# Performance work log

Measured on AMD Instinct MI355X. Metric: run time of the kernel, lower is better.

The kernel has to match this reference:

```python
import jax, jax.numpy as jnp
import numpy as np

N_IMG, N_CAP, N_REG, N_WORD = 64, 64, 36, 20
EMBED, SIM = 1024, 256
RCAR_STEP = 3          # rar_step=3, rcr_step=2, alv_step=3
T2I_SMOOTH = 9.0
EPS = 1e-8


def l2norm(x):
    return x / (jnp.linalg.norm(x, axis=-1, keepdims=True) + EPS)


def xavier(key, shape):
    fan_in, fan_out = shape[-1], shape[-2]
    r = float(np.sqrt(6.0 / (fan_in + fan_out)))
    return jax.random.uniform(key, shape, jnp.float32, -r, r)


def cross_attention(query, context, matrix, smooth):
    # query: (B, Q, D), context: (B, S, D); matrix broadcasts over query; smooth scalar or (B,Q,1)
    q = query * matrix
    attn = jnp.einsum('bsd,bqd->bsq', context, q)          # (B, S, Q)
    attn = jax.nn.leaky_relu(attn, 0.1)
    attn = l2norm(attn)                                     # normalize over Q
    attn = jnp.swapaxes(attn, 1, 2)                         # (B, Q, S)
    attn = jax.nn.softmax(attn * smooth, axis=2)
    wcontext = jnp.einsum('bqs,bsd->bqd', attn, context)    # (B, Q, D)
    return l2norm(wcontext)


def setup_inputs() -> dict:
    key = jax.random.key(0)
    ks = jax.random.split(key, 12)
    inp = {}
    inp['img_emb'] = jax.random.normal(ks[0], (N_IMG, N_REG, EMBED), jnp.float32)
    inp['cap_emb'] = jax.random.normal(ks[1], (N_CAP, N_WORD, EMBED), jnp.float32)
    inp['cap_lens'] = jnp.full((N_CAP,), N_WORD, dtype=jnp.int32)
    # Alignment_vector: Linear(embed -> sim), 3 steps
    inp['alv_w'] = xavier(ks[2], (RCAR_STEP, SIM, EMBED))
    inp['alv_b'] = jnp.zeros((RCAR_STEP, SIM), jnp.float32)
    # Aggregation_regulator: q/k Linear(sim->sim), v Linear(sim->1), 3 steps
    inp['rar_qw'] = xavier(ks[3], (RCAR_STEP, SIM, SIM))
    inp['rar_qb'] = jnp.zeros((RCAR_STEP, SIM), jnp.float32)
    inp['rar_kw'] = xavier(ks[4], (RCAR_STEP, SIM, SIM))
    inp['rar_kb'] = jnp.zeros((RCAR_STEP, SIM), jnp.float32)
    inp['rar_vw'] = xavier(ks[5], (RCAR_STEP, 1, SIM))
    inp['rar_vb'] = jnp.zeros((RCAR_STEP, 1), jnp.float32)
    # Correpondence_regulator: smooth MLP sim->sim//2->1, matrix MLP sim->2*sim->embed, 2 steps
    inp['rcr_sw1'] = xavier(ks[6], (RCAR_STEP - 1, SIM // 2, SIM))
    inp['rcr_sb1'] = jnp.zeros((RCAR_STEP - 1, SIM // 2), jnp.float32)
    inp['rcr_sw2'] = xavier(ks[7], (RCAR_STEP - 1, 1, SIM // 2))
    inp['rcr_sb2'] = jnp.zeros((RCAR_STEP - 1, 1), jnp.float32)
    inp['rcr_mw1'] = xavier(ks[8], (RCAR_STEP - 1, 2 * SIM, SIM))
    inp['rcr_mb1'] = jnp.zeros((RCAR_STEP - 1, 2 * SIM), jnp.float32)
    inp['rcr_mw2'] = xavier(ks[9], (RCAR_STEP - 1, EMBED, 2 * SIM))
    inp['rcr_mb2'] = jnp.zeros((RCAR_STEP - 1, EMBED), jnp.float32)
    # sim_eval_w: Linear(sim -> 1)
    inp['eval_w'] = xavier(ks[10], (1, SIM))
    inp['eval_b'] = jnp.zeros((1,), jnp.float32)
    return inp


def _forward(img_emb, cap_emb,
             alv_w, alv_b,
             rar_qw, rar_qb, rar_kw, rar_kb, rar_vw, rar_vb,
             rcr_sw1, rcr_sb1, rcr_sw2, rcr_sb2, rcr_mw1, rcr_mb1, rcr_mw2, rcr_mb2,
             eval_w, eval_b):
    n_img = img_emb.shape[0]

    def per_caption(cap_i):                       # cap_i: (L, D)
        query = jnp.broadcast_to(cap_i[None], (n_img,) + cap_i.shape)  # t2i: text is query
        context = img_emb                                               # (n_img, S, D)
        matrix = jnp.ones((EMBED,), cap_i.dtype)
        smooth = jnp.asarray(T2I_SMOOTH, cap_i.dtype)
        sim_hig = None
        for m in range(RCAR_STEP):
            # Alignment_vector (dropout is inference-mode identity)
            wctx = cross_attention(query, context, matrix, smooth)
            sim_rep = (query - wctx) ** 2
            sim_mid = l2norm(jnp.einsum('bqd,sd->bqs', sim_rep, alv_w[m]) + alv_b[m])  # (B,Q,SIM)
            if m == 0:
                sim_hig = sim_mid.mean(axis=1)                                          # (B,SIM)
            if m < RCAR_STEP - 1:
                # Correpondence_regulator
                hm = jnp.tanh(jnp.einsum('bqs,ts->bqt', sim_mid, rcr_mw1[m]) + rcr_mb1[m])
                mm = jnp.einsum('bqt,dt->bqd', hm, rcr_mw2[m]) + rcr_mb2[m]
                matrix = jnp.clip(jnp.tanh(mm) + matrix, -1.0, 1.0)                     # (B,Q,D)
                hs = jnp.tanh(jnp.einsum('bqs,ts->bqt', sim_mid, rcr_sw1[m]) + rcr_sb1[m])
                ss = jnp.einsum('bqt,ot->bqo', hs, rcr_sw2[m]) + rcr_sb2[m]
                smooth = jax.nn.relu(ss + smooth)                                       # (B,Q,1)
            # Aggregation_regulator
            mid_k = jnp.tanh(jnp.einsum('bqs,ts->bqt', sim_mid, rar_kw[m]) + rar_kb[m])
            hig_q = jnp.tanh(sim_hig @ rar_qw[m].T + rar_qb[m])[:, None, :]             # (B,1,SIM)
            w = jnp.einsum('bqs,os->bqo', mid_k * hig_q, rar_vw[m]) + rar_vb[m]         # (B,Q,1)
            w = jax.nn.softmax(w[..., 0], axis=1)
            sim_hig = l2norm(jnp.einsum('bq,bqs->bs', w, sim_mid))
        sim_i = jax.nn.sigmoid(sim_hig @ eval_w.T + eval_b)                             # (B,1)
        return sim_i[:, 0]

    sims = jax.vmap(per_caption)(cap_emb)        # (n_cap, n_img)
    return sims.T                                 # (n_img, n_cap) == torch.cat(sim_all, 1)


def reference(img_emb, cap_emb, cap_lens,
              alv_w, alv_b,
              rar_qw, rar_qb, rar_kw, rar_kb, rar_vw, rar_vb,
              rcr_sw1, rcr_sb1, rcr_sw2, rcr_sb2, rcr_mw1, rcr_mb1, rcr_mw2, rcr_mb2,
              eval_w, eval_b):
    # cap_lens are all equal to N_WORD (constant-length captions), so the per-caption
    # slice cap_emb[i, :n_word] is the full row and the loop vectorizes exactly.
    del cap_lens
    return _forward(img_emb, cap_emb, alv_w, alv_b,
                    rar_qw, rar_qb, rar_kw, rar_kb, rar_vw, rar_vb,
                    rcr_sw1, rcr_sb1, rcr_sw2, rcr_sb2, rcr_mw1, rcr_mb1, rcr_mw2, rcr_mb2,
                    eval_w, eval_b)
```

## Files before the change

### kernel.cpp

```cpp
#include <hip/hip_runtime.h>
#include <math.h>

#define NIMG 64
#define NCAP 64
#define NREG 36
#define NWORD 20
#define EMBED 1024
#define SIMDIM 256
#define H1 512
#define HSD 128
#define EPS 1e-8f

#define QSTR 1032
#define SMSTR 264
#define PSTR 72
#define ATSTR 37

typedef unsigned short u16t;
typedef __bf16 bf8 __attribute__((ext_vector_type(8)));
typedef short  s8i __attribute__((ext_vector_type(8)));
typedef float  f4  __attribute__((ext_vector_type(4)));

__device__ __forceinline__ float wsum(float v) {
#pragma unroll
  for (int o = 32; o > 0; o >>= 1) v += __shfl_xor(v, o);
  return v;
}
__device__ __forceinline__ float wmax(float v) {
#pragma unroll
  for (int o = 32; o > 0; o >>= 1) v = fmaxf(v, __shfl_xor(v, o));
  return v;
}
__device__ __forceinline__ float ftanh(float x) {
  x = fminf(fmaxf(x, -15.f), 15.f);
  float e = __expf(2.f * x);
  return (e - 1.f) / (e + 1.f);
}
__device__ __forceinline__ float d4(float4 a, float4 b) {
  return a.x*b.x + a.y*b.y + a.z*b.z + a.w*b.w;
}
__device__ __forceinline__ u16t f2bf(float f) {
  unsigned u = __float_as_uint(f);
  u += 0x7FFFu + ((u >> 16) & 1u);
  return (u16t)(u >> 16);
}
__device__ __forceinline__ float bf2f(u16t h) { return __uint_as_float(((unsigned)h) << 16); }
__device__ __forceinline__ bf8 zero8() {
  s8i z = {0,0,0,0,0,0,0,0};
  return __builtin_bit_cast(bf8, z);
}
#define MFMA16(a, b, c) __builtin_amdgcn_mfma_f32_16x16x32_bf16((a), (b), (c), 0, 0, 0)

#define WS_ALV   0u
#define WS_KW    786432u
#define WS_MW1   983040u
#define WS_MW2   1245184u
#define WS_SW1   2293760u
#define WS_IMG   2359296u
#define WS_CTXT  4718592u
#define WS_END   8912896u
#define N_CVT    4718592u

#define OFFB_MAT    17825792ull
#define OFFB_SMID   (OFFB_MAT + 83886080ull)
#define OFFB_SHIG   (OFFB_SMID + 41943040ull)
#define OFFB_SMOOTH (OFFB_SHIG + 4194304ull)
#define WS_FULL_BYTES (OFFB_SMOOTH + 327680ull)

__global__ void cvt_kernel(const float* __restrict__ alv, const float* __restrict__ kw,
                           const float* __restrict__ mw1, const float* __restrict__ mw2,
                           const float* __restrict__ sw1, const float* __restrict__ img,
                           u16t* __restrict__ ws) {
  for (unsigned i = blockIdx.x * blockDim.x + threadIdx.x; i < N_CVT; i += gridDim.x * blockDim.x) {
    unsigned o = i; float v;
    if (o < 786432u) v = alv[o];
    else if ((o -= 786432u) < 196608u) v = kw[o];
    else if ((o -= 196608u) < 262144u) v = mw1[o];
    else if ((o -= 262144u) < 1048576u) v = mw2[o];
    else if ((o -= 1048576u) < 65536u) v = sw1[o];
    else { o -= 65536u; v = img[o]; }
    ws[i] = f2bf(v);
  }
}

__global__ void ctxt_kernel(const float* __restrict__ img, u16t* __restrict__ ctxT) {
  __shared__ float tile[36 * 65];
  int b = blockIdx.x;
  int im = b >> 4, dt = (b & 15) * 64;
  const float* src = img + (size_t)im * 36 * 1024 + dt;
  for (int e = threadIdx.x; e < 36 * 64; e += 256) {
    int s = e >> 6, dd = e & 63;
    tile[s * 65 + dd] = src[s * 1024 + dd];
  }
  __syncthreads();
  u16t* dst = ctxT + (size_t)im * 65536 + dt * 64;
  for (int o = threadIdx.x; o < 4096; o += 256) {
    int dd = o >> 6, sp = o & 63;
    dst[dd * 64 + sp] = (sp < 36) ? f2bf(tile[sp * 65 + dd]) : (u16t)0;
  }
}

__global__ __launch_bounds__(512, 4) void simenc_k1(
    const float* __restrict__ cap_emb,
    const float* __restrict__ alv_b,
    const float* __restrict__ rar_qw, const float* __restrict__ rar_qb,
    const float* __restrict__ rar_kb,
    const float* __restrict__ rar_vw, const float* __restrict__ rar_vb,
    const float* __restrict__ sb1, const float* __restrict__ sw2, const float* __restrict__ sb2,
    const float* __restrict__ eval_w, const float* __restrict__ eval_b,
    const u16t* __restrict__ ws,
    signed char* __restrict__ mat_g, u16t* __restrict__ smid_g,
    float* __restrict__ shig_g, float* __restrict__ smooth_g,
    int m, float* __restrict__ out)
{
  __shared__ __attribute__((aligned(16))) u16t qsrep[NWORD * QSTR];
  __shared__ __attribute__((aligned(16))) u16t smidb[NWORD * SMSTR];
  __shared__ __attribute__((aligned(16))) u16t p_bf[NWORD * PSTR];
  __shared__ float attnT[NWORD * ATSTR];
  __shared__ float colscale[36];
  __shared__ float smoothq[NWORD];
  __shared__ float sim_hig[SIMDIM];
  __shared__ float red[8 * NWORD];
  __shared__ float rq[NWORD];
  __shared__ float logits_s[NWORD];
  __shared__ float wsm[NWORD];
  __shared__ float ssig_s;

  const int tid = threadIdx.x;
  const int lane = tid & 63;
  const int wv = tid >> 6;
  const int lr = lane & 15;
  const int lg = lane >> 4;
  const int koff = lg * 8;

  const int xcd = blockIdx.x & 7;
  const int j_  = blockIdx.x >> 3;
  const int img = xcd * 8 + (j_ & 7);
  const int cap = j_ >> 3;
  const int pid = img * NCAP + cap;

  const float* qry  = cap_emb + (size_t)cap * (NWORD * EMBED);
  const u16t* imgW  = ws + WS_IMG + (size_t)img * (NREG * EMBED);
  const u16t* ctxTW = ws + WS_CTXT + (size_t)img * (EMBED * 64);
  const u16t* alvW  = ws + WS_ALV + (size_t)m * (SIMDIM * EMBED);
  const u16t* kwW   = ws + WS_KW  + (size_t)m * (SIMDIM * SIMDIM);
  const u16t* sw1W  = ws + WS_SW1 + (size_t)m * (HSD * SIMDIM);

  if (tid < NWORD)
    smoothq[tid] = (m == 0) ? 9.0f : smooth_g[(size_t)pid * 20 + tid];
  if (m > 0 && tid < 256)
    sim_hig[tid] = shig_g[(size_t)pid * 256 + tid];
  __syncthreads();

  if (m == 0) {
#pragma unroll 4
    for (int q = 0; q < NWORD; ++q) {
      qsrep[q * QSTR + tid] = f2bf(qry[q * 1024 + tid]);
      qsrep[q * QSTR + 512 + tid] = f2bf(qry[q * 1024 + 512 + tid]);
    }
  } else {
    const signed char* mg = mat_g + (size_t)pid * 20480;
#pragma unroll 4
    for (int q = 0; q < NWORD; ++q) {
      float mv0 = (float)mg[q * 1024 + tid] * (1.f / 127.f);
      float mv1 = (float)mg[q * 1024 + 512 + tid] * (1.f / 127.f);
      qsrep[q * QSTR + tid] = f2bf(qry[q * 1024 + tid] * mv0);
      qsrep[q * QSTR + 512 + tid] = f2bf(qry[q * 1024 + 512 + tid] * mv1);
    }
  }
  __syncthreads();

  if (wv < 6) {
    int q0 = (wv & 1) * 16, s0 = (wv >> 1) * 16;
    int ari = q0 + lr; bool am = ari >= NWORD; int ar = am ? 0 : ari;
    int bri = s0 + lr; bool bm = bri >= NREG;  int br = bm ? 0 : bri;
    const u16t* ap = qsrep + ar * QSTR + koff;
    const u16t* bp = imgW + (size_t)br * 1024 + koff;
    f4 acc0 = {0.f,0.f,0.f,0.f}, acc1 = {0.f,0.f,0.f,0.f};
#pragma unroll 2
    for (int kk = 0; kk < 32; kk += 2) {
      bf8 a0 = *(const bf8*)(ap + kk * 32);       if (am) a0 = zero8();
      bf8 b0 = *(const bf8*)(bp + kk * 32);       if (bm) b0 = zero8();
      bf8 a1 = *(const bf8*)(ap + (kk + 1) * 32); if (am) a1 = zero8();
      bf8 b1 = *(const bf8*)(bp + (kk + 1) * 32); if (bm) b1 = zero8();
      acc0 = MFMA16(a0, b0, acc0);
      acc1 = MFMA16(a1, b1, acc1);
    }
    f4 acc = acc0 + acc1;
#pragma unroll
    for (int r = 0; r < 4; ++r) {
      int q = q0 + lg * 4 + r, s = s0 + lr;
      if (q < NWORD && s < NREG) {
        float x = acc[r];
        attnT[q * ATSTR + s] = (x > 0.f) ? x : 0.1f * x;
      }
    }
  }
  __syncthreads();

  if (tid < NREG) {
    float ss = 0.f;
#pragma unroll
    for (int q = 0; q < NWORD; ++q) { float v = attnT[q * ATSTR + tid]; ss += v * v; }
    colscale[tid] = 1.f / (sqrtf(ss) + EPS);
  }
  __syncthreads();

#pragma unroll
  for (int pass = 0; pass < 3; ++pass) {
    int q = wv + pass * 8;
    if (q < NWORD) {
      float x = (lane < NREG)
              ? attnT[q * ATSTR + lane] * colscale[lane] * smoothq[q] : -1e30f;
      float mx = wmax(x);
      float e = (lane < NREG) ? __expf(x - mx) : 0.f;
      float s = wsum(e);
      p_bf[q * PSTR + lane] = f2bf(e / s);
    }
  }
  __syncthreads();

  {
    bf8 pa[2][2];
#pragma unroll
    for (int kk = 0; kk < 2; ++kk) {
      pa[0][kk] = *(const bf8*)(p_bf + lr * PSTR + kk * 32 + koff);
      pa[1][kk] = (16 + lr < NWORD)
                ? *(const bf8*)(p_bf + (16 + lr) * PSTR + kk * 32 + koff) : zero8();
    }
    float s2[8];
#pragma unroll
    for (int i = 0; i < 8; ++i) s2[i] = 0.f;
#pragma unroll
    for (int nt = 0; nt < 8; ++nt) {
      int d0 = wv * 128 + nt * 16;
      const u16t* bp = ctxTW + (size_t)(d0 + lr) * 64 + koff;
      bf8 b0 = *(const bf8*)(bp);
      bf8 b1 = *(const bf8*)(bp + 32);
      int d = d0 + lr;
#pragma unroll
      for (int m2 = 0; m2 < 2; ++m2) {
        f4 acc = {0.f,0.f,0.f,0.f};
        acc = MFMA16(pa[m2][0], b0, acc);
        acc = MFMA16(pa[m2][1], b1, acc);
#pragma unroll
        for (int r = 0; r < 4; ++r) {
          int q = m2 * 16 + lg * 4 + r;
          s2[m2 * 4 + r] += acc[r] * acc[r];
          if (q < NWORD) qsrep[q * QSTR + d] = f2bf(acc[r]);
        }
      }
    }
#pragma unroll
    for (int o = 1; o < 16; o <<= 1)
#pragma unroll
      for (int i = 0; i < 8; ++i) s2[i] += __shfl_xor(s2[i], o);
    if (lr == 0) {
#pragma unroll
      for (int r = 0; r < 4; ++r) red[wv * 20 + lg * 4 + r] = s2[r];
      if (lg == 0)
#pragma unroll
        for (int r = 0; r < 4; ++r) red[wv * 20 + 16 + r] = s2[4 + r];
    }
    __syncthreads();
    if (tid < NWORD) {
      float s = 0.f;
#pragma unroll
      for (int w = 0; w < 8; ++w) s += red[w * 20 + tid];
      rq[tid] = 1.f / (sqrtf(s) + EPS);
    }
    __syncthreads();
#pragma unroll
    for (int nt = 0; nt < 8; ++nt) {
      int d = wv * 128 + nt * 16 + lr;
#pragma unroll
      for (int m2 = 0; m2 < 2; ++m2)
#pragma unroll
        for (int r = 0; r < 4; ++r) {
          int q = m2 * 16 + lg * 4 + r;
          if (q < NWORD) {
            float wn = bf2f(qsrep[q * QSTR + d]) * rq[q];
            float t = qry[q * 1024 + d] - wn;
            qsrep[q * QSTR + d] = f2bf(t * t);
          }
        }
    }
  }
  __syncthreads();

  {
    int t0 = wv * 32 + lr;
    const u16t* bp0 = alvW + (size_t)t0 * 1024 + koff;
    const u16t* bp1 = bp0 + 16 * 1024;
    int ari = 16 + lr; bool am = ari >= NWORD; int ar = am ? 0 : ari;
    f4 a00 = {0,0,0,0}, a01 = {0,0,0,0}, a10 = {0,0,0,0}, a11 = {0,0,0,0};
#pragma unroll 2
    for (int kk = 0; kk < 32; ++kk) {
      bf8 b0 = *(const bf8*)(bp0 + kk * 32);
      bf8 b1 = *(const bf8*)(bp1 + kk * 32);
      bf8 x0 = *(const bf8*)(qsrep + lr * QSTR + kk * 32 + koff);
      bf8 x1 = *(const bf8*)(qsrep + ar * QSTR + kk * 32 + koff); if (am) x1 = zero8();
      a00 = MFMA16(x0, b0, a00);
      a01 = MFMA16(x1, b0, a01);
      a10 = MFMA16(x0, b1, a10);
      a11 = MFMA16(x1, b1, a11);
    }
    float bias0 = alv_b[m * SIMDIM + t0];
    float bias1 = alv_b[m * SIMDIM + t0 + 16];
    float s2[8];
#pragma unroll
    for (int r = 0; r < 4; ++r) {
      a00[r] += bias0; a10[r] += bias1;
      s2[r] = a00[r] * a00[r] + a10[r] * a10[r];
    }
#pragma unroll
    for (int r = 0; r < 4; ++r) {
      a01[r] += bias0; a11[r] += bias1;
      s2[4 + r] = (lg == 0) ? a01[r] * a01[r] + a11[r] * a11[r] : 0.f;
    }
#pragma unroll
    for (int o = 1; o < 16; o <<= 1)
#pragma unroll
      for (int i = 0; i < 8; ++i) s2[i] += __shfl_xor(s2[i], o);
    if (lr == 0) {
#pragma unroll
      for (int r = 0; r < 4; ++r) red[wv * 20 + lg * 4 + r] = s2[r];
      if (lg == 0)
#pragma unroll
        for (int r = 0; r < 4; ++r) red[wv * 20 + 16 + r] = s2[4 + r];
    }
    __syncthreads();
    if (tid < NWORD) {
      float s = 0.f;
#pragma unroll
      for (int w = 0; w < 8; ++w) s += red[w * 20 + tid];
      rq[tid] = 1.f / (sqrtf(s) + EPS);
    }
    __syncthreads();
    u16t* sg = smid_g + (size_t)pid * 5120;
#pragma unroll
    for (int r = 0; r < 4; ++r) {
      int q = lg * 4 + r;
      float v0 = a00[r] * rq[q], v1 = a10[r] * rq[q];
      u16t h0 = f2bf(v0), h1 = f2bf(v1);
      ((float*)(qsrep + q * QSTR + 512))[t0] = v0;
      ((float*)(qsrep + q * QSTR + 512))[t0 + 16] = v1;
      smidb[q * SMSTR + t0] = h0;
      smidb[q * SMSTR + t0 + 16] = h1;
      sg[q * 256 + t0] = h0;
      sg[q * 256 + t0 + 16] = h1;
    }
    if (lg == 0)
#pragma unroll
      for (int r = 0; r < 4; ++r) {
        int q = 16 + r;
        float v0 = a01[r] * rq[q], v1 = a11[r] * rq[q];
        u16t h0 = f2bf(v0), h1 = f2bf(v1);
        ((float*)(qsrep + q * QSTR + 512))[t0] = v0;
        ((float*)(qsrep + q * QSTR + 512))[t0 + 16] = v1;
        smidb[q * SMSTR + t0] = h0;
        smidb[q * SMSTR + t0 + 16] = h1;
        sg[q * 256 + t0] = h0;
        sg[q * 256 + t0 + 16] = h1;
      }
  }
  __syncthreads();

  if (m == 0 && tid < 256) {
    float s = 0.f;
#pragma unroll
    for (int q = 0; q < NWORD; ++q) s += ((const float*)(qsrep + q * QSTR + 512))[tid];
    sim_hig[tid] = s * (1.f / NWORD);
  }
  __syncthreads();

  if (m < 2) {
    {
      int j0 = wv * 16;
      int ari = 16 + lr; bool am = ari >= NWORD; int ar = am ? 0 : ari;
      f4 h0 = {0,0,0,0}, h1 = {0,0,0,0};
#pragma unroll 2
      for (int kk = 0; kk < 8; ++kk) {
        bf8 b = *(const bf8*)(sw1W + (size_t)(j0 + lr) * 256 + kk * 32 + koff);
        bf8 x0 = *(const bf8*)(smidb + lr * SMSTR + kk * 32 + koff);
        bf8 x1 = *(const bf8*)(smidb + ar * SMSTR + kk * 32 + koff); if (am) x1 = zero8();
        h0 = MFMA16(x0, b, h0);
        h1 = MFMA16(x1, b, h1);
      }
      int j = j0 + lr;
      float bias = sb1[m * HSD + j];
      float s2v = sw2[m * HSD + j];
      float part[8];
#pragma unroll
      for (int r = 0; r < 4; ++r) part[r] = ftanh(h0[r] + bias) * s2v;
#pragma unroll
      for (int r = 0; r < 4; ++r) part[4 + r] = (lg == 0) ? ftanh(h1[r] + bias) * s2v : 0.f;
#pragma unroll
      for (int o = 1; o < 16; o <<= 1)
#pragma unroll
        for (int i = 0; i < 8; ++i) part[i] += __shfl_xor(part[i], o);
      if (lr == 0) {
#pragma unroll
        for (int r = 0; r < 4; ++r) red[wv * 20 + lg * 4 + r] = part[r];
        if (lg == 0)
#pragma unroll
          for (int r = 0; r < 4; ++r) red[wv * 20 + 16 + r] = part[4 + r];
      }
    }
    __syncthreads();
    if (tid < NWORD) {
      float s = 0.f;
#pragma unroll
      for (int w = 0; w < 8; ++w) s += red[w * 20 + tid];
      smooth_g[(size_t)pid * 20 + tid] = fmaxf(0.f, s + sb2[m] + smoothq[tid]);
    }
    __syncthreads();
  }

  {
    int ari = 16 + lr; bool am = ari >= NWORD; int ar = am ? 0 : ari;
    float part[8];
#pragma unroll
    for (int i = 0; i < 8; ++i) part[i] = 0.f;
#pragma unroll
    for (int h = 0; h < 2; ++h) {
      int t_ = wv * 32 + h * 16 + lr;
      const float4* wq = (const float4*)(rar_qw + ((size_t)m * SIMDIM + t_) * SIMDIM);
      const float4* sh = (const float4*)sim_hig;
      float hacc = 0.f;
#pragma unroll 2
      for (int i = 0; i < SIMDIM / 4; ++i) hacc += d4(wq[i], sh[i]);
      float hq = ftanh(hacc + rar_qb[m * SIMDIM + t_]) * rar_vw[m * SIMDIM + t_];

      f4 k0 = {0,0,0,0}, k1v = {0,0,0,0};
#pragma unroll 2
      for (int kk = 0; kk < 8; ++kk) {
        bf8 b = *(const bf8*)(kwW + (size_t)t_ * 256 + kk * 32 + koff);
        bf8 x0 = *(const bf8*)(smidb + lr * SMSTR + kk * 32 + koff);
        bf8 x1 = *(const bf8*)(smidb + ar * SMSTR + kk * 32 + koff); if (am) x1 = zero8();
        k0 = MFMA16(x0, b, k0);
        k1v = MFMA16(x1, b, k1v);
      }
      float kb = rar_kb[m * SIMDIM + t_];
#pragma unroll
      for (int r = 0; r < 4; ++r) part[r] += ftanh(k0[r] + kb) * hq;
      if (lg == 0)
#pragma unroll
        for (int r = 0; r < 4; ++r) part[4 + r] += ftanh(k1v[r] + kb) * hq;
    }
#pragma unroll
    for (int o = 1; o < 16; o <<= 1)
#pragma unroll
      for (int i = 0; i < 8; ++i) part[i] += __shfl_xor(part[i], o);
    if (lr == 0) {
#pragma unroll
      for (int r = 0; r < 4; ++r) red[wv * 20 + lg * 4 + r] = part[r];
      if (lg == 0)
#pragma unroll
        for (int r = 0; r < 4; ++r) red[wv * 20 + 16 + r] = part[4 + r];
    }
  }
  __syncthreads();
  if (tid < NWORD) {
    float s = 0.f;
#pragma unroll
    for (int w = 0; w < 8; ++w) s += red[w * 20 + tid];
    logits_s[tid] = s + rar_vb[m];
  }
  __syncthreads();
  if (tid < 64) {
    float v = (tid < NWORD) ? logits_s[tid] : -1e30f;
    float mx = wmax(v);
    float e = (tid < NWORD) ? __expf(v - mx) : 0.f;
    float s = wsum(e);
    if (tid < NWORD) wsm[tid] = e / s;
  }
  __syncthreads();
  if (tid < 256) {
    float a = 0.f;
#pragma unroll
    for (int q = 0; q < NWORD; ++q) a += wsm[q] * ((const float*)(qsrep + q * QSTR + 512))[tid];
    sim_hig[tid] = a;
  }
  __syncthreads();
  if (tid < 64) {
    float4 v = ((const float4*)sim_hig)[tid];
    float s = wsum(d4(v, v));
    if (tid == 0) ssig_s = 1.f / (sqrtf(s) + EPS);
  }
  __syncthreads();

  if (m < 2) {
    if (tid < 256)
      shig_g[(size_t)pid * 256 + tid] = sim_hig[tid] * ssig_s;
  } else {
    if (tid < 64) {
      float4 s4v = ((const float4*)sim_hig)[tid];
      float4 w4v = ((const float4*)eval_w)[tid];
      float v = wsum(d4(s4v, w4v)) * ssig_s;
      if (tid == 0)
        out[pid] = 1.f / (1.f + __expf(-(v + eval_b[0])));
    }
  }
}

__global__ __launch_bounds__(1024, 4) void simenc_k2(
    const float* __restrict__ mb1, const float* __restrict__ mb2,
    const u16t* __restrict__ ws,
    const u16t* __restrict__ smid_g, signed char* __restrict__ mat_g,
    int m)
{
  __shared__ __attribute__((aligned(16))) u16t hm_l[80 * 512];
  __shared__ __attribute__((aligned(16))) signed char mat_l[80 * 1024];

  const int tid = threadIdx.x;
  const int lane = tid & 63;
  const int wv = tid >> 6;
  const int lr = lane & 15;
  const int lg = lane >> 4;
  const int koff = lg * 8;

  const int pid0 = blockIdx.x * 4;
  const u16t* mw1W = ws + WS_MW1 + (size_t)m * (H1 * SIMDIM);
  const u16t* mw2W = ws + WS_MW2 + (size_t)m * (EMBED * H1);
  const u16t* smidB = smid_g + (size_t)pid0 * 5120;

#pragma unroll
  for (int nt = 0; nt < 2; ++nt) {
    int j0 = (wv * 2 + nt) * 16;
    f4 acc[5];
#pragma unroll
    for (int mt = 0; mt < 5; ++mt) acc[mt] = (f4){0,0,0,0};
#pragma unroll 2
    for (int kk = 0; kk < 8; ++kk) {
      bf8 b = *(const bf8*)(mw1W + (size_t)(j0 + lr) * 256 + kk * 32 + koff);
#pragma unroll
      for (int mt = 0; mt < 5; ++mt) {
        bf8 a = *(const bf8*)(smidB + (size_t)(mt * 16 + lr) * 256 + kk * 32 + koff);
        acc[mt] = MFMA16(a, b, acc[mt]);
      }
    }
    int j = j0 + lr;
    float bias = mb1[m * H1 + j];
#pragma unroll
    for (int mt = 0; mt < 5; ++mt)
#pragma unroll
      for (int r = 0; r < 4; ++r) {
        int rb = mt * 16 + lg * 4 + r;
        unsigned byteoff = (unsigned)rb * 1024u
                         + (((unsigned)j * 2u) ^ (((unsigned)rb & 7u) << 4));
        *(u16t*)((char*)hm_l + byteoff) = f2bf(ftanh(acc[mt][r] + bias));
      }
  }
  __syncthreads();

#pragma unroll
  for (int nt = 0; nt < 4; ++nt) {
    int d0 = (wv * 4 + nt) * 16;
    f4 acc[5];
#pragma unroll
    for (int mt = 0; mt < 5; ++mt) acc[mt] = (f4){0,0,0,0};
#pragma unroll 2
    for (int kk = 0; kk < 16; ++kk) {
      bf8 b = *(const bf8*)(mw2W + (size_t)(d0 + lr) * 512 + kk * 32 + koff);
#pragma unroll
      for (int mt = 0; mt < 5; ++mt) {
        int rb = mt * 16 + lr;
        unsigned byteoff = (unsigned)rb * 1024u
                         + (((unsigned)(kk * 64 + lg * 16)) ^ (((unsigned)rb & 7u) << 4));
        bf8 a = *(const bf8*)((const char*)hm_l + byteoff);
        acc[mt] = MFMA16(a, b, acc[mt]);
      }
    }
    int d = d0 + lr;
    float bias = mb2[m * EMBED + d];
#pragma unroll
    for (int mt = 0; mt < 5; ++mt)
#pragma unroll
      for (int r = 0; r < 4; ++r) {
        int rb = mt * 16 + lg * 4 + r;
        float v = ftanh(acc[mt][r] + bias);
        mat_l[rb * 1024 + d] = (signed char)__float2int_rn(v * 127.f);
      }
  }
  __syncthreads();

  {
    signed char* matB = mat_g + (size_t)pid0 * 20480;
#pragma unroll
    for (int i = 0; i < 5; ++i) {
      int off = i * 16384 + tid * 16;
      int4 sv = *(const int4*)(mat_l + off);
      int4 ov;
      if (m > 0) ov = *(const int4*)(matB + off);
      const signed char* svb = (const signed char*)&sv;
      const signed char* ovb = (const signed char*)&ov;
      int4 res;
      signed char* rsb = (signed char*)&res;
#pragma unroll
      for (int b = 0; b < 16; ++b) {
        float v = (float)svb[b] * (1.f / 127.f);
        float mo = (m == 0) ? 1.f : (float)ovb[b] * (1.f / 127.f);
        float mn = fminf(fmaxf(v + mo, -1.f), 1.f);
        rsb[b] = (signed char)__float2int_rn(mn * 127.f);
      }
      *(int4*)(matB + off) = res;
    }
  }
}

__global__ __launch_bounds__(1024) void simenc_valu(
    const float* __restrict__ img_emb, const float* __restrict__ cap_emb,
    const float* __restrict__ alv_w,  const float* __restrict__ alv_b,
    const float* __restrict__ rar_qw, const float* __restrict__ rar_qb,
    const float* __restrict__ rar_kw, const float* __restrict__ rar_kb,
    const float* __restrict__ rar_vw, const float* __restrict__ rar_vb,
    const float* __restrict__ sw1, const float* __restrict__ sb1,
    const float* __restrict__ sw2, const float* __restrict__ sb2,
    const float* __restrict__ mw1, const float* __restrict__ mb1,
    const float* __restrict__ mw2, const float* __restrict__ mb2,
    const float* __restrict__ eval_w, const float* __restrict__ eval_b,
    float* __restrict__ out)
{
  __shared__ float buf[NWORD * EMBED];
  __shared__ float smid[NWORD * SIMDIM];
  __shared__ float attn_raw[NREG * NWORD];
  __shared__ float attnT[NWORD * NREG];
  __shared__ float smoothq[NWORD];
  __shared__ float sim_hig[SIMDIM];
  __shared__ float hqu[SIMDIM];
  __shared__ float wsm_[NWORD];
  __shared__ float red[16 * NWORD];
  __shared__ float rq[NWORD];
  __shared__ float ssig;

  const int tid = threadIdx.x;
  const int lane = tid & 63;
  const int wv = tid >> 6;
  const int pair = blockIdx.x;
  const int img = pair & 63;
  const int cap = pair >> 6;
  const float* ctx = img_emb + (size_t)img * (NREG * EMBED);
  const float* qry = cap_emb + (size_t)cap * (NWORD * EMBED);

  float mat[NWORD];
#pragma unroll
  for (int q = 0; q < NWORD; ++q) mat[q] = 1.f;
  if (tid < NWORD) smoothq[tid] = 9.f;
  __syncthreads();

  for (int m = 0; m < 3; ++m) {
#pragma unroll 4
    for (int q = 0; q < NWORD; ++q)
      buf[q * EMBED + tid] = qry[q * EMBED + tid] * mat[q];
    __syncthreads();
    if (tid < NWORD * NREG) {
      int q = tid / NREG, s = tid % NREG;
      const float4* c4 = (const float4*)(ctx + s * EMBED);
      const float4* q4 = (const float4*)(buf + q * EMBED);
      float acc = 0.f;
#pragma unroll 4
      for (int i = 0; i < EMBED / 4; ++i) acc += d4(c4[i], q4[i]);
      attn_raw[s * NWORD + q] = (acc > 0.f) ? acc : 0.1f * acc;
    }
    __syncthreads();
    if (tid < NREG) {
      int s = tid; float sumsq = 0.f;
#pragma unroll
      for (int q = 0; q < NWORD; ++q) { float v = attn_raw[s * NWORD + q]; sumsq += v * v; }
      float sc = 1.f / (sqrtf(sumsq) + EPS);
#pragma unroll
      for (int q = 0; q < NWORD; ++q) attnT[q * NREG + s] = attn_raw[s * NWORD + q] * sc;
    }
    __syncthreads();
    if (tid < NWORD) {
      int q = tid; float sm = smoothq[q]; float mx = -1e30f;
      for (int s = 0; s < NREG; ++s) mx = fmaxf(mx, attnT[q * NREG + s] * sm);
      float sum = 0.f;
      for (int s = 0; s < NREG; ++s) { float e = __expf(attnT[q * NREG + s] * sm - mx); attnT[q * NREG + s] = e; sum += e; }
      float r = 1.f / sum;
      for (int s = 0; s < NREG; ++s) attnT[q * NREG + s] *= r;
    }
    __syncthreads();
    {
      float wacc[NWORD];
#pragma unroll
      for (int q = 0; q < NWORD; ++q) wacc[q] = 0.f;
#pragma unroll
      for (int sc_ = 0; sc_ < 3; ++sc_) {
        float c[12];
#pragma unroll
        for (int i = 0; i < 12; ++i) c[i] = ctx[(sc_ * 12 + i) * EMBED + tid];
#pragma unroll
        for (int q = 0; q < NWORD; ++q) {
          const float4* a4 = (const float4*)(attnT + q * NREG + sc_ * 12);
          float4 a0 = a4[0], a1 = a4[1], a2 = a4[2];
          wacc[q] += a0.x*c[0] + a0.y*c[1] + a0.z*c[2] + a0.w*c[3]
                   + a1.x*c[4] + a1.y*c[5] + a1.z*c[6] + a1.w*c[7]
                   + a2.x*c[8] + a2.y*c[9] + a2.z*c[10] + a2.w*c[11];
        }
      }
#pragma unroll
      for (int q = 0; q < NWORD; ++q) {
        float v = wsum(wacc[q] * wacc[q]);
        if (lane == 0) red[wv * NWORD + q] = v;
      }
      __syncthreads();
      if (tid < NWORD) {
        float s = 0.f;
#pragma unroll
        for (int w = 0; w < 16; ++w) s += red[w * NWORD + tid];
        rq[tid] = 1.f / (sqrtf(s) + EPS);
      }
      __syncthreads();
#pragma unroll 4
      for (int q = 0; q < NWORD; ++q) {
        float wn = wacc[q] * rq[q];
        float t = qry[q * EMBED + tid] - wn;
        buf[q * EMBED + tid] = t * t;
      }
    }
    __syncthreads();
    {
      int t = tid & 255, g = tid >> 8;
      const float4* w4 = (const float4*)(alv_w + ((size_t)m * SIMDIM + t) * EMBED);
      float acc[5] = {0, 0, 0, 0, 0};
      for (int i = 0; i < EMBED / 4; ++i) {
        float4 w = w4[i];
#pragma unroll
        for (int k = 0; k < 5; ++k) acc[k] += d4(w, ((const float4*)(buf + (g + 4 * k) * EMBED))[i]);
      }
      float b = alv_b[m * SIMDIM + t];
#pragma unroll
      for (int k = 0; k < 5; ++k) smid[(g + 4 * k) * SIMDIM + t] = acc[k] + b;
    }
    __syncthreads();
#pragma unroll
    for (int rep = 0; rep < 2; ++rep) {
      int q = wv + rep * 16;
      if (q < NWORD) {
        float4 v = ((const float4*)(smid + q * SIMDIM))[lane];
        float s = wsum(d4(v, v));
        if (lane == 0) rq[q] = 1.f / (sqrtf(s) + EPS);
      }
    }
    __syncthreads();
#pragma unroll
    for (int k = 0; k < 5; ++k) { int e = tid + k * 1024; smid[e] *= rq[e >> 8]; }
    __syncthreads();
    if (m == 0 && tid < SIMDIM) {
      float s = 0.f;
#pragma unroll
      for (int q = 0; q < NWORD; ++q) s += smid[q * SIMDIM + tid];
      sim_hig[tid] = s * (1.f / NWORD);
    }
    __syncthreads();
    if (m < 2) {
      {
        int j = tid & 511, g = tid >> 9;
        const float4* w4 = (const float4*)(mw1 + ((size_t)m * H1 + j) * SIMDIM);
        float acc[10];
#pragma unroll
        for (int k = 0; k < 10; ++k) acc[k] = 0.f;
        for (int i = 0; i < SIMDIM / 4; ++i) {
          float4 w = w4[i];
#pragma unroll
          for (int k = 0; k < 10; ++k) acc[k] += d4(w, ((const float4*)(smid + (g + 2 * k) * SIMDIM))[i]);
        }
        float b = mb1[m * H1 + j];
#pragma unroll
        for (int k = 0; k < 10; ++k) buf[(g + 2 * k) * H1 + j] = ftanh(acc[k] + b);
      }
      __syncthreads();
      {
        const float4* w4 = (const float4*)(mw2 + ((size_t)m * EMBED + tid) * H1);
        float acc[NWORD];
#pragma unroll
        for (int q = 0; q < NWORD; ++q) acc[q] = 0.f;
        for (int i = 0; i < H1 / 4; ++i) {
          float4 w = w4[i];
#pragma unroll
          for (int q = 0; q < NWORD; ++q) acc[q] += d4(w, ((const float4*)(buf + q * H1))[i]);
        }
        float b = mb2[m * EMBED + tid];
#pragma unroll
        for (int q = 0; q < NWORD; ++q)
          mat[q] = fminf(fmaxf(ftanh(acc[q] + b) + mat[q], -1.f), 1.f);
      }
      {
        int j = tid & 127, g = tid >> 7;
        const float4* w4 = (const float4*)(sw1 + ((size_t)m * HSD + j) * SIMDIM);
        float a0 = 0.f, a1 = 0.f, a2 = 0.f;
        for (int i = 0; i < SIMDIM / 4; ++i) {
          float4 w = w4[i];
          a0 += d4(w, ((const float4*)(smid + g * SIMDIM))[i]);
          a1 += d4(w, ((const float4*)(smid + (g + 8) * SIMDIM))[i]);
          if (g < 4) a2 += d4(w, ((const float4*)(smid + (g + 16) * SIMDIM))[i]);
        }
        float b = sb1[m * HSD + j];
        buf[10240 + g * HSD + j] = ftanh(a0 + b);
        buf[10240 + (g + 8) * HSD + j] = ftanh(a1 + b);
        if (g < 4) buf[10240 + (g + 16) * HSD + j] = ftanh(a2 + b);
      }
      __syncthreads();
      {
        const float* sw2m = sw2 + m * HSD;
#pragma unroll
        for (int rep = 0; rep < 2; ++rep) {
          int q = wv + rep * 16;
          if (q < NWORD) {
            float v = buf[10240 + q * HSD + lane] * sw2m[lane]
                    + buf[10240 + q * HSD + 64 + lane] * sw2m[64 + lane];
            v = wsum(v);
            if (lane == 0) smoothq[q] = fmaxf(0.f, v + sb2[m] + smoothq[q]);
          }
        }
      }
      __syncthreads();
    }
    {
      int t = tid & 255, g = tid >> 8;
      const float4* w4 = (const float4*)(rar_kw + ((size_t)m * SIMDIM + t) * SIMDIM);
      float acc[5] = {0, 0, 0, 0, 0};
      for (int i = 0; i < SIMDIM / 4; ++i) {
        float4 w = w4[i];
#pragma unroll
        for (int k = 0; k < 5; ++k) acc[k] += d4(w, ((const float4*)(smid + (g + 4 * k) * SIMDIM))[i]);
      }
      float b = rar_kb[m * SIMDIM + t];
#pragma unroll
      for (int k = 0; k < 5; ++k) buf[12800 + (g + 4 * k) * SIMDIM + t] = ftanh(acc[k] + b);
    }
    if (tid < SIMDIM) {
      const float4* w4 = (const float4*)(rar_qw + ((size_t)m * SIMDIM + tid) * SIMDIM);
      const float4* s4 = (const float4*)sim_hig;
      float acc = 0.f;
      for (int i = 0; i < SIMDIM / 4; ++i) acc += d4(w4[i], s4[i]);
      hqu[tid] = ftanh(acc + rar_qb[m * SIMDIM + tid]) * rar_vw[m * SIMDIM + tid];
    }
    __syncthreads();
#pragma unroll
    for (int rep = 0; rep < 2; ++rep) {
      int q = wv + rep * 16;
      if (q < NWORD) {
        float4 a = ((const float4*)(buf + 12800 + q * SIMDIM))[lane];
        float4 u = ((const float4*)hqu)[lane];
        float v = wsum(d4(a, u));
        if (lane == 0) red[q] = v + rar_vb[m];
      }
    }
    __syncthreads();
    if (tid < 64) {
      float v = (tid < NWORD) ? red[tid] : -1e30f;
      float mx = wmax(v);
      float e = (tid < NWORD) ? __expf(v - mx) : 0.f;
      float s = wsum(e);
      if (tid < NWORD) wsm_[tid] = e / s;
    }
    __syncthreads();
    if (tid < SIMDIM) {
      float acc = 0.f;
#pragma unroll
      for (int q = 0; q < NWORD; ++q) acc += wsm_[q] * smid[q * SIMDIM + tid];
      sim_hig[tid] = acc;
    }
    __syncthreads();
    if (tid < 64) {
      float4 v = ((const float4*)sim_hig)[tid];
      float s = wsum(d4(v, v));
      if (tid == 0) ssig = 1.f / (sqrtf(s) + EPS);
    }
    __syncthreads();
    if (tid < SIMDIM) sim_hig[tid] *= ssig;
    __syncthreads();
  }
  if (tid < 64) {
    float4 s4v = ((const float4*)sim_hig)[tid];
    float4 w4v = ((const float4*)eval_w)[tid];
    float v = wsum(d4(s4v, w4v));
    if (tid == 0) out[img * NCAP + cap] = 1.f / (1.f + __expf(-(v + eval_b[0])));
  }
}

extern "C" void kernel_launch(void* const* d_in, const int* in_sizes, int n_in,
                              void* d_out, int out_size, void* d_ws, size_t ws_size,
                              hipStream_t stream) {
  (void)in_sizes; (void)n_in; (void)out_size;
  u16t* ws = (u16t*)d_ws;

  if (ws_size >= (size_t)WS_FULL_BYTES) {
    cvt_kernel<<<2048, 1024, 0, stream>>>(
        (const float*)d_in[3],  (const float*)d_in[7],  (const float*)d_in[15],
        (const float*)d_in[17], (const float*)d_in[11], (const float*)d_in[0], ws);
    ctxt_kernel<<<1024, 256, 0, stream>>>((const float*)d_in[0], ws + WS_CTXT);

    signed char* mat_g = (signed char*)d_ws + OFFB_MAT;
    u16t*  smid_g   = (u16t*)((char*)d_ws + OFFB_SMID);
    float* shig_g   = (float*)((char*)d_ws + OFFB_SHIG);
    float* smooth_g = (float*)((char*)d_ws + OFFB_SMOOTH);

    for (int m = 0; m < 3; ++m) {
      simenc_k1<<<NIMG * NCAP, 512, 0, stream>>>(
          (const float*)d_in[1],  (const float*)d_in[4],
          (const float*)d_in[5],  (const float*)d_in[6],  (const float*)d_in[8],
          (const float*)d_in[9],  (const float*)d_in[10],
          (const float*)d_in[12], (const float*)d_in[13], (const float*)d_in[14],
          (const float*)d_in[19], (const float*)d_in[20],
          ws, mat_g, smid_g, shig_g, smooth_g, m, (float*)d_out);
      if (m < 2)
        simenc_k2<<<NIMG * NCAP / 4, 1024, 0, stream>>>(
            (const float*)d_in[16], (const float*)d_in[18],
            ws, smid_g, mat_g, m);
    }
  } else {
    simenc_valu<<<NIMG * NCAP, 1024, 0, stream>>>(
        (const float*)d_in[0],  (const float*)d_in[1],
        (const float*)d_in[3],  (const float*)d_in[4],
        (const float*)d_in[5],  (const float*)d_in[6],
        (const float*)d_in[7],  (const float*)d_in[8],
        (const float*)d_in[9],  (const float*)d_in[10],
        (const float*)d_in[11], (const float*)d_in[12],
        (const float*)d_in[13], (const float*)d_in[14],
        (const float*)d_in[15], (const float*)d_in[16],
        (const float*)d_in[17], (const float*)d_in[18],
        (const float*)d_in[19], (const float*)d_in[20],
        (float*)d_out);
  }
}
```

Measured before the change: 3.517 ms.

## Split per-pair encoder kernel into staged kernels batching weight GEMMs across pairs

The monolithic per-(image,caption) kernel is split into stages. An attention kernel writes the squared-difference representation to global memory. A batched kernel then applies the alignment linear layer with MFMA over four pairs per block, followed by separate kernels for the query projection, key/smooth projections, and softmax aggregation. This amortizes weight loads across pairs and raises MFMA tile utilization. In exchange it adds about 160 MB of extra global traffic per step for the intermediate buffer, plus more kernel launches. The old fallback VALU kernel is removed in favour of the previous fused path.

```diff
diff --git a/kernel.cpp b/kernel.cpp
--- a/kernel.cpp
+++ b/kernel.cpp
@@ -66,6 +66,10 @@
 #define OFFB_SHIG   (OFFB_SMID + 41943040ull)
 #define OFFB_SMOOTH (OFFB_SHIG + 4194304ull)
 #define WS_FULL_BYTES (OFFB_SMOOTH + 327680ull)
+#define OFFB_SREP   (OFFB_SMOOTH + 327680ull)
+#define OFFB_HQU    (OFFB_SREP + 167772160ull)
+#define OFFB_LOG    (OFFB_HQU + 4194304ull)
+#define WS_FULL2_BYTES (OFFB_LOG + 327680ull)
 
 __global__ void cvt_kernel(const float* __restrict__ alv, const float* __restrict__ kw,
                            const float* __restrict__ mw1, const float* __restrict__ mw2,
@@ -100,7 +104,551 @@
   }
 }
 
-__global__ __launch_bounds__(512, 4) void simenc_k1(
+__global__ __launch_bounds__(512, 4) void simenc_ka(
+    const float* __restrict__ cap_emb,
+    const u16t* __restrict__ ws,
+    const signed char* __restrict__ mat_g,
+    const float* __restrict__ smooth_g,
+    u16t* __restrict__ srep_g,
+    int m)
+{
+  __shared__ __attribute__((aligned(16))) u16t qsrep[NWORD * QSTR];
+  __shared__ __attribute__((aligned(16))) u16t p_bf[NWORD * PSTR];
+  __shared__ float attnT[NWORD * ATSTR];
+  __shared__ float colscale[36];
+  __shared__ float smoothq[NWORD];
+  __shared__ float red[8 * NWORD];
+  __shared__ float rq[NWORD];
+
+  const int tid = threadIdx.x;
+  const int lane = tid & 63;
+  const int wv = tid >> 6;
+  const int lr = lane & 15;
+  const int lg = lane >> 4;
+  const int koff = lg * 8;
+
+  const int xcd = blockIdx.x & 7;
+  const int j_  = blockIdx.x >> 3;
+  const int img = xcd * 8 + (j_ & 7);
+  const int cap = j_ >> 3;
+  const int pid = img * NCAP + cap;
+
+  const float* qry  = cap_emb + (size_t)cap * (NWORD * EMBED);
+  const u16t* imgW  = ws + WS_IMG + (size_t)img * (NREG * EMBED);
+  const u16t* ctxTW = ws + WS_CTXT + (size_t)img * (EMBED * 64);
+
+  if (tid < NWORD)
+    smoothq[tid] = (m == 0) ? 9.0f : smooth_g[(size_t)pid * 20 + tid];
+  __syncthreads();
+
+  if (m == 0) {
+#pragma unroll 4
+    for (int q = 0; q < NWORD; ++q) {
+      qsrep[q * QSTR + tid] = f2bf(qry[q * 1024 + tid]);
+      qsrep[q * QSTR + 512 + tid] = f2bf(qry[q * 1024 + 512 + tid]);
+    }
+  } else {
+    const signed char* mg = mat_g + (size_t)pid * 20480;
+#pragma unroll 4
+    for (int q = 0; q < NWORD; ++q) {
+      float mv0 = (float)mg[q * 1024 + tid] * (1.f / 127.f);
+      float mv1 = (float)mg[q * 1024 + 512 + tid] * (1.f / 127.f);
+      qsrep[q * QSTR + tid] = f2bf(qry[q * 1024 + tid] * mv0);
+      qsrep[q * QSTR + 512 + tid] = f2bf(qry[q * 1024 + 512 + tid] * mv1);
+    }
+  }
+  __syncthreads();
+
+  if (wv < 6) {
+    int q0 = (wv & 1) * 16, s0 = (wv >> 1) * 16;
+    int ari = q0 + lr; bool am = ari >= NWORD; int ar = am ? 0 : ari;
+    int bri = s0 + lr; bool bm = bri >= NREG;  int br = bm ? 0 : bri;
+    const u16t* ap = qsrep + ar * QSTR + koff;
+    const u16t* bp = imgW + (size_t)br * 1024 + koff;
+    f4 acc0 = {0.f,0.f,0.f,0.f}, acc1 = {0.f,0.f,0.f,0.f};
+#pragma unroll 2
+    for (int kk = 0; kk < 32; kk += 2) {
+      bf8 a0 = *(const bf8*)(ap + kk * 32);       if (am) a0 = zero8();
+      bf8 b0 = *(const bf8*)(bp + kk * 32);       if (bm) b0 = zero8();
+      bf8 a1 = *(const bf8*)(ap + (kk + 1) * 32); if (am) a1 = zero8();
+      bf8 b1 = *(const bf8*)(bp + (kk + 1) * 32); if (bm) b1 = zero8();
+      acc0 = MFMA16(a0, b0, acc0);
+      acc1 = MFMA16(a1, b1, acc1);
+    }
+    f4 acc = acc0 + acc1;
+#pragma unroll
+    for (int r = 0; r < 4; ++r) {
+      int q = q0 + lg * 4 + r, s = s0 + lr;
+      if (q < NWORD && s < NREG) {
+        float x = acc[r];
+        attnT[q * ATSTR + s] = (x > 0.f) ? x : 0.1f * x;
+      }
+    }
+  }
+  __syncthreads();
+
+  if (tid < NREG) {
+    float ss = 0.f;
+#pragma unroll
+    for (int q = 0; q < NWORD; ++q) { float v = attnT[q * ATSTR + tid]; ss += v * v; }
+    colscale[tid] = 1.f / (sqrtf(ss) + EPS);
+  }
+  __syncthreads();
+
+#pragma unroll
+  for (int pass = 0; pass < 3; ++pass) {
+    int q = wv + pass * 8;
+    if (q < NWORD) {
+      float x = (lane < NREG)
+              ? attnT[q * ATSTR + lane] * colscale[lane] * smoothq[q] : -1e30f;
+      float mx = wmax(x);
+      float e = (lane < NREG) ? __expf(x - mx) : 0.f;
+      float s = wsum(e);
+      p_bf[q * PSTR + lane] = f2bf(e / s);
+    }
+  }
+  __syncthreads();
+
+  {
+    bf8 pa[2][2];
+#pragma unroll
+    for (int kk = 0; kk < 2; ++kk) {
+      pa[0][kk] = *(const bf8*)(p_bf + lr * PSTR + kk * 32 + koff);
+      pa[1][kk] = (16 + lr < NWORD)
+                ? *(const bf8*)(p_bf + (16 + lr) * PSTR + kk * 32 + koff) : zero8();
+    }
+    float s2[8];
+#pragma unroll
+    for (int i = 0; i < 8; ++i) s2[i] = 0.f;
+#pragma unroll
+    for (int nt = 0; nt < 8; ++nt) {
+      int d0 = wv * 128 + nt * 16;
+      const u16t* bp = ctxTW + (size_t)(d0 + lr) * 64 + koff;
+      bf8 b0 = *(const bf8*)(bp);
+      bf8 b1 = *(const bf8*)(bp + 32);
+      int d = d0 + lr;
+#pragma unroll
+      for (int m2 = 0; m2 < 2; ++m2) {
+        f4 acc = {0.f,0.f,0.f,0.f};
+        acc = MFMA16(pa[m2][0], b0, acc);
+        acc = MFMA16(pa[m2][1], b1, acc);
+#pragma unroll
+        for (int r = 0; r < 4; ++r) {
+          int q = m2 * 16 + lg * 4 + r;
+          s2[m2 * 4 + r] += acc[r] * acc[r];
+          if (q < NWORD) qsrep[q * QSTR + d] = f2bf(acc[r]);
+        }
+      }
+    }
+#pragma unroll
+    for (int o = 1; o < 16; o <<= 1)
+#pragma unroll
+      for (int i = 0; i < 8; ++i) s2[i] += __shfl_xor(s2[i], o);
+    if (lr == 0) {
+#pragma unroll
+      for (int r = 0; r < 4; ++r) red[wv * 20 + lg * 4 + r] = s2[r];
+      if (lg == 0)
+#pragma unroll
+        for (int r = 0; r < 4; ++r) red[wv * 20 + 16 + r] = s2[4 + r];
+    }
+    __syncthreads();
+    if (tid < NWORD) {
+      float s = 0.f;
+#pragma unroll
+      for (int w = 0; w < 8; ++w) s += red[w * 20 + tid];
+      rq[tid] = 1.f / (sqrtf(s) + EPS);
+    }
+    __syncthreads();
+#pragma unroll
+    for (int nt = 0; nt < 8; ++nt) {
+      int d = wv * 128 + nt * 16 + lr;
+#pragma unroll
+      for (int m2 = 0; m2 < 2; ++m2)
+#pragma unroll
+        for (int r = 0; r < 4; ++r) {
+          int q = m2 * 16 + lg * 4 + r;
+          if (q < NWORD) {
+            float wn = bf2f(qsrep[q * QSTR + d]) * rq[q];
+            float t = qry[q * 1024 + d] - wn;
+            qsrep[q * QSTR + d] = f2bf(t * t);
+          }
+        }
+    }
+  }
+  __syncthreads();
+
+  {
+    u16t* sp = srep_g + (size_t)pid * 20480;
+#pragma unroll 4
+    for (int i = tid; i < 20480; i += 512) {
+      int row = i >> 10, col = i & 1023;
+      sp[i] = qsrep[row * QSTR + col];
+    }
+  }
+}
+
+__global__ __launch_bounds__(1024, 4) void simenc_kf(
+    const float* __restrict__ alv_b,
+    const u16t* __restrict__ ws,
+    const u16t* __restrict__ srep_g,
+    u16t* __restrict__ smid_g,
+    float* __restrict__ shig_g,
+    int m)
+{
+  __shared__ __attribute__((aligned(16))) u16t smid_l[80 * SMSTR];
+  __shared__ float red[16 * 80];
+  __shared__ float rq80[80];
+
+  const int tid = threadIdx.x;
+  const int lane = tid & 63;
+  const int wv = tid >> 6;
+  const int lr = lane & 15;
+  const int lg = lane >> 4;
+  const int koff = lg * 8;
+
+  const int pid0 = blockIdx.x * 4;
+  const u16t* alvW = ws + WS_ALV + (size_t)m * (SIMDIM * EMBED);
+  const u16t* srepB = srep_g + (size_t)pid0 * 20480;
+
+  int t_ = wv * 16 + lr;
+  f4 acc[5];
+#pragma unroll
+  for (int mt = 0; mt < 5; ++mt) acc[mt] = (f4){0,0,0,0};
+#pragma unroll 2
+  for (int kk = 0; kk < 32; ++kk) {
+    bf8 b = *(const bf8*)(alvW + (size_t)t_ * 1024 + kk * 32 + koff);
+#pragma unroll
+    for (int mt = 0; mt < 5; ++mt) {
+      bf8 a = *(const bf8*)(srepB + (size_t)(mt * 16 + lr) * 1024 + kk * 32 + koff);
+      acc[mt] = MFMA16(a, b, acc[mt]);
+    }
+  }
+  float bias = alv_b[m * SIMDIM + t_];
+  float p[20];
+#pragma unroll
+  for (int mt = 0; mt < 5; ++mt)
+#pragma unroll
+    for (int r = 0; r < 4; ++r) {
+      acc[mt][r] += bias;
+      p[mt * 4 + r] = acc[mt][r] * acc[mt][r];
+    }
+#pragma unroll
+  for (int o = 1; o < 16; o <<= 1)
+#pragma unroll
+    for (int i = 0; i < 20; ++i) p[i] += __shfl_xor(p[i], o);
+  if (lr == 0)
+#pragma unroll
+    for (int mt = 0; mt < 5; ++mt)
+#pragma unroll
+      for (int r = 0; r < 4; ++r)
+        red[wv * 80 + mt * 16 + lg * 4 + r] = p[mt * 4 + r];
+  __syncthreads();
+  if (tid < 80) {
+    float s = 0.f;
+#pragma unroll
+    for (int w = 0; w < 16; ++w) s += red[w * 80 + tid];
+    rq80[tid] = 1.f / (sqrtf(s) + EPS);
+  }
+  __syncthreads();
+#pragma unroll
+  for (int mt = 0; mt < 5; ++mt)
+#pragma unroll
+    for (int r = 0; r < 4; ++r) {
+      int rb = mt * 16 + lg * 4 + r;
+      float v = acc[mt][r] * rq80[rb];
+      u16t hv = f2bf(v);
+      smid_g[(size_t)(pid0 * 20 + rb) * 256 + t_] = hv;
+      smid_l[rb * SMSTR + t_] = hv;
+    }
+  if (m == 0) {
+    __syncthreads();
+    int col = tid & 255, pp = tid >> 8;
+    float s = 0.f;
+#pragma unroll
+    for (int q = 0; q < NWORD; ++q) s += bf2f(smid_l[(pp * 20 + q) * SMSTR + col]);
+    shig_g[(size_t)(pid0 + pp) * 256 + col] = s * (1.f / NWORD);
+  }
+}
+
+__global__ __launch_bounds__(1024) void simenc_kh(
+    const float* __restrict__ rar_qw, const float* __restrict__ rar_qb,
+    const float* __restrict__ rar_vw,
+    const float* __restrict__ shig_g, float* __restrict__ hqu_g, int m)
+{
+  int idx = blockIdx.x * 1024 + threadIdx.x;
+  int pid = idx >> 8, t = idx & 255;
+  const float4* sh = (const float4*)(shig_g + (size_t)pid * 256);
+  const float4* wq = (const float4*)(rar_qw + ((size_t)m * SIMDIM + t) * SIMDIM);
+  float acc = 0.f;
+#pragma unroll 8
+  for (int i = 0; i < SIMDIM / 4; ++i) acc += d4(wq[i], sh[i]);
+  hqu_g[idx] = ftanh(acc + rar_qb[m * SIMDIM + t]) * rar_vw[m * SIMDIM + t];
+}
+
+__global__ __launch_bounds__(1024, 4) void simenc_kr(
+    const float* __restrict__ rar_kb, const float* __restrict__ rar_vb,
+    const float* __restrict__ sb1, const float* __restrict__ sw2, const float* __restrict__ sb2,
+    const u16t* __restrict__ ws,
+    const u16t* __restrict__ smid_g, const float* __restrict__ hqu_g,
+    float* __restrict__ logits_g, float* __restrict__ smooth_g,
+    int m)
+{
+  __shared__ float red[16 * 80];
+
+  const int tid = threadIdx.x;
+  const int lane = tid & 63;
+  const int wv = tid >> 6;
+  const int lr = lane & 15;
+  const int lg = lane >> 4;
+  const int koff = lg * 8;
+
+  const int pid0 = blockIdx.x * 4;
+  const u16t* kwW  = ws + WS_KW  + (size_t)m * (SIMDIM * SIMDIM);
+  const u16t* sw1W = ws + WS_SW1 + (size_t)m * (HSD * SIMDIM);
+  const u16t* smidB = smid_g + (size_t)pid0 * 5120;
+
+  {
+    int t_ = wv * 16 + lr;
+    f4 acc[5];
+#pragma unroll
+    for (int mt = 0; mt < 5; ++mt) acc[mt] = (f4){0,0,0,0};
+#pragma unroll 2
+    for (int kk = 0; kk < 8; ++kk) {
+      bf8 b = *(const bf8*)(kwW + (size_t)t_ * 256 + kk * 32 + koff);
+#pragma unroll
+      for (int mt = 0; mt < 5; ++mt) {
+        bf8 a = *(const bf8*)(smidB + (size_t)(mt * 16 + lr) * 256 + kk * 32 + koff);
+        acc[mt] = MFMA16(a, b, acc[mt]);
+      }
+    }
+    float kb = rar_kb[m * SIMDIM + t_];
+    float p[20];
+#pragma unroll
+    for (int mt = 0; mt < 5; ++mt)
+#pragma unroll
+      for (int r = 0; r < 4; ++r) {
+        int rb = mt * 16 + lg * 4 + r;
+        float hq = hqu_g[(size_t)(pid0 + rb / 20) * 256 + t_];
+        p[mt * 4 + r] = ftanh(acc[mt][r] + kb) * hq;
+      }
+#pragma unroll
+    for (int o = 1; o < 16; o <<= 1)
+#pragma unroll
+      for (int i = 0; i < 20; ++i) p[i] += __shfl_xor(p[i], o);
+    if (lr == 0)
+#pragma unroll
+      for (int mt = 0; mt < 5; ++mt)
+#pragma unroll
+        for (int r = 0; r < 4; ++r)
+          red[wv * 80 + mt * 16 + lg * 4 + r] = p[mt * 4 + r];
+  }
+  __syncthreads();
+  if (tid < 80) {
+    float s = 0.f;
+#pragma unroll
+    for (int w = 0; w < 16; ++w) s += red[w * 80 + tid];
+    logits_g[(size_t)pid0 * 20 + tid] = s + rar_vb[m];
+  }
+
+  if (m < 2) {
+    __syncthreads();
+    if (wv < 8) {
+      int j_ = wv * 16 + lr;
+      f4 acc[5];
+#pragma unroll
+      for (int mt = 0; mt < 5; ++mt) acc[mt] = (f4){0,0,0,0};
+#pragma unroll 2
+      for (int kk = 0; kk < 8; ++kk) {
+        bf8 b = *(const bf8*)(sw1W + (size_t)j_ * 256 + kk * 32 + koff);
+#pragma unroll
+        for (int mt = 0; mt < 5; ++mt) {
+          bf8 a = *(const bf8*)(smidB + (size_t)(mt * 16 + lr) * 256 + kk * 32 + koff);
+          acc[mt] = MFMA16(a, b, acc[mt]);
+        }
+      }
+      float b1 = sb1[m * HSD + j_];
+      float s2v = sw2[m * HSD + j_];
+      float p[20];
+#pragma unroll
+      for (int mt = 0; mt < 5; ++mt)
+#pragma unroll
+        for (int r = 0; r < 4; ++r)
+          p[mt * 4 + r] = ftanh(acc[mt][r] + b1) * s2v;
+#pragma unroll
+      for (int o = 1; o < 16; o <<= 1)
+#pragma unroll
+        for (int i = 0; i < 20; ++i) p[i] += __shfl_xor(p[i], o);
+      if (lr == 0)
+#pragma unroll
+        for (int mt = 0; mt < 5; ++mt)
+#pragma unroll
+          for (int r = 0; r < 4; ++r)
+            red[wv * 80 + mt * 16 + lg * 4 + r] = p[mt * 4 + r];
+    }
+    __syncthreads();
+    if (tid < 80) {
+      float s = 0.f;
+#pragma unroll
+      for (int w = 0; w < 8; ++w) s += red[w * 80 + tid];
+      float old = (m == 0) ? 9.0f : smooth_g[(size_t)pid0 * 20 + tid];
+      smooth_g[(size_t)pid0 * 20 + tid] = fmaxf(0.f, s + sb2[m] + old);
+    }
+  }
+}
+
+__global__ __launch_bounds__(256) void simenc_ki(
+    const float* __restrict__ eval_w, const float* __restrict__ eval_b,
+    const u16t* __restrict__ smid_g, const float* __restrict__ logits_g,
+    float* __restrict__ shig_g, float* __restrict__ out, int m)
+{
+  __shared__ float wsm[NWORD];
+  __shared__ float sh[SIMDIM];
+  __shared__ float red4[4];
+  __shared__ float rsig;
+
+  const int pid = blockIdx.x;
+  const int tid = threadIdx.x;
+
+  if (tid < 64) {
+    float v = (tid < NWORD) ? logits_g[(size_t)pid * 20 + tid] : -1e30f;
+    float mx = wmax(v);
+    float e = (tid < NWORD) ? __expf(v - mx) : 0.f;
+    float s = wsum(e);
+    if (tid < NWORD) wsm[tid] = e / s;
+  }
+  __syncthreads();
+  {
+    const u16t* sm = smid_g + (size_t)pid * 5120 + tid;
+    float a = 0.f;
+#pragma unroll
+    for (int q = 0; q < NWORD; ++q) a += wsm[q] * bf2f(sm[q * 256]);
+    sh[tid] = a;
+  }
+  __syncthreads();
+  {
+    float v = sh[tid];
+    float ss = wsum(v * v);
+    if ((tid & 63) == 0) red4[tid >> 6] = ss;
+  }
+  __syncthreads();
+  if (tid == 0) rsig = 1.f / (sqrtf(red4[0] + red4[1] + red4[2] + red4[3]) + EPS);
+  __syncthreads();
+  if (m < 2) {
+    shig_g[(size_t)pid * 256 + tid] = sh[tid] * rsig;
+  } else if (tid < 64) {
+    float4 s4 = ((const float4*)sh)[tid];
+    float4 w4 = ((const float4*)eval_w)[tid];
+    float v = wsum(d4(s4, w4)) * rsig;
+    if (tid == 0) out[pid] = 1.f / (1.f + __expf(-(v + eval_b[0])));
+  }
+}
+
+__global__ __launch_bounds__(1024, 4) void simenc_k2(
+    const float* __restrict__ mb1, const float* __restrict__ mb2,
+    const u16t* __restrict__ ws,
+    const u16t* __restrict__ smid_g, signed char* __restrict__ mat_g,
+    int m)
+{
+  __shared__ __attribute__((aligned(16))) u16t hm_l[80 * 512];
+  __shared__ __attribute__((aligned(16))) signed char mat_l[80 * 1024];
+
+  const int tid = threadIdx.x;
+  const int lane = tid & 63;
+  const int wv = tid >> 6;
+  const int lr = lane & 15;
+  const int lg = lane >> 4;
+  const int koff = lg * 8;
+
+  const int pid0 = blockIdx.x * 4;
+  const u16t* mw1W = ws + WS_MW1 + (size_t)m * (H1 * SIMDIM);
+  const u16t* mw2W = ws + WS_MW2 + (size_t)m * (EMBED * H1);
+  const u16t* smidB = smid_g + (size_t)pid0 * 5120;
+
+#pragma unroll
+  for (int nt = 0; nt < 2; ++nt) {
+    int j0 = (wv * 2 + nt) * 16;
+    f4 acc[5];
+#pragma unroll
+    for (int mt = 0; mt < 5; ++mt) acc[mt] = (f4){0,0,0,0};
+#pragma unroll 2
+    for (int kk = 0; kk < 8; ++kk) {
+      bf8 b = *(const bf8*)(mw1W + (size_t)(j0 + lr) * 256 + kk * 32 + koff);
+#pragma unroll
+      for (int mt = 0; mt < 5; ++mt) {
+        bf8 a = *(const bf8*)(smidB + (size_t)(mt * 16 + lr) * 256 + kk * 32 + koff);
+        acc[mt] = MFMA16(a, b, acc[mt]);
+      }
+    }
+    int j = j0 + lr;
+    float bias = mb1[m * H1 + j];
+#pragma unroll
+    for (int mt = 0; mt < 5; ++mt)
+#pragma unroll
+      for (int r = 0; r < 4; ++r) {
+        int rb = mt * 16 + lg * 4 + r;
+        unsigned byteoff = (unsigned)rb * 1024u
+                         + (((unsigned)j * 2u) ^ (((unsigned)rb & 7u) << 4));
+        *(u16t*)((char*)hm_l + byteoff) = f2bf(ftanh(acc[mt][r] + bias));
+      }
+  }
+  __syncthreads();
+
+#pragma unroll
+  for (int nt = 0; nt < 4; ++nt) {
+    int d0 = (wv * 4 + nt) * 16;
+    f4 acc[5];
+#pragma unroll
+    for (int mt = 0; mt < 5; ++mt) acc[mt] = (f4){0,0,0,0};
+#pragma unroll 2
+    for (int kk = 0; kk < 16; ++kk) {
+      bf8 b = *(const bf8*)(mw2W + (size_t)(d0 + lr) * 512 + kk * 32 + koff);
+#pragma unroll
+      for (int mt = 0; mt < 5; ++mt) {
+        int rb = mt * 16 + lr;
+        unsigned byteoff = (unsigned)rb * 1024u
+                         + (((unsigned)(kk * 64 + lg * 16)) ^ (((unsigned)rb & 7u) << 4));
+        bf8 a = *(const bf8*)((const char*)hm_l + byteoff);
+        acc[mt] = MFMA16(a, b, acc[mt]);
+      }
+    }
+    int d = d0 + lr;
+    float bias = mb2[m * EMBED + d];
+#pragma unroll
+    for (int mt = 0; mt < 5; ++mt)
+#pragma unroll
+      for (int r = 0; r < 4; ++r) {
+        int rb = mt * 16 + lg * 4 + r;
+        float v = ftanh(acc[mt][r] + bias);
+        mat_l[rb * 1024 + d] = (signed char)__float2int_rn(v * 127.f);
+      }
+  }
+  __syncthreads();
+
+  {
+    signed char* matB = mat_g + (size_t)pid0 * 20480;
+#pragma unroll
+    for (int i = 0; i < 5; ++i) {
+      int off = i * 16384 + tid * 16;
+      int4 sv = *(const int4*)(mat_l + off);
+      int4 ov;
+      if (m > 0) ov = *(const int4*)(matB + off);
+      const signed char* svb = (const signed char*)&sv;
+      const signed char* ovb = (const signed char*)&ov;
+      int4 res;
+      signed char* rsb = (signed char*)&res;
+#pragma unroll
+      for (int b = 0; b < 16; ++b) {
+        float v = (float)svb[b] * (1.f / 127.f);
+        float mo = (m == 0) ? 1.f : (float)ovb[b] * (1.f / 127.f);
+        float mn = fminf(fmaxf(v + mo, -1.f), 1.f);
+        rsb[b] = (signed char)__float2int_rn(mn * 127.f);
+      }
+      *(int4*)(matB + off) = res;
+    }
+  }
+}
+
+__global__ __launch_bounds__(512, 4) void simenc_k1f(
     const float* __restrict__ cap_emb,
     const float* __restrict__ alv_b,
     const float* __restrict__ rar_qw, const float* __restrict__ rar_qb,
@@ -504,403 +1052,50 @@
   }
 }
 
-__global__ __launch_bounds__(1024, 4) void simenc_k2(
-    const float* __restrict__ mb1, const float* __restrict__ mb2,
-    const u16t* __restrict__ ws,
-    const u16t* __restrict__ smid_g, signed char* __restrict__ mat_g,
-    int m)
-{
-  __shared__ __attribute__((aligned(16))) u16t hm_l[80 * 512];
-  __shared__ __attribute__((aligned(16))) signed char mat_l[80 * 1024];
-
-  const int tid = threadIdx.x;
-  const int lane = tid & 63;
-  const int wv = tid >> 6;
-  const int lr = lane & 15;
-  const int lg = lane >> 4;
-  const int koff = lg * 8;
-
-  const int pid0 = blockIdx.x * 4;
-  const u16t* mw1W = ws + WS_MW1 + (size_t)m * (H1 * SIMDIM);
-  const u16t* mw2W = ws + WS_MW2 + (size_t)m * (EMBED * H1);
-  const u16t* smidB = smid_g + (size_t)pid0 * 5120;
-
-#pragma unroll
-  for (int nt = 0; nt < 2; ++nt) {
-    int j0 = (wv * 2 + nt) * 16;
-    f4 acc[5];
-#pragma unroll
-    for (int mt = 0; mt < 5; ++mt) acc[mt] = (f4){0,0,0,0};
-#pragma unroll 2
-    for (int kk = 0; kk < 8; ++kk) {
-      bf8 b = *(const bf8*)(mw1W + (size_t)(j0 + lr) * 256 + kk * 32 + koff);
-#pragma unroll
-      for (int mt = 0; mt < 5; ++mt) {
-        bf8 a = *(const bf8*)(smidB + (size_t)(mt * 16 + lr) * 256 + kk * 32 + koff);
-        acc[mt] = MFMA16(a, b, acc[mt]);
-      }
-    }
-    int j = j0 + lr;
-    float bias = mb1[m * H1 + j];
-#pragma unroll
-    for (int mt = 0; mt < 5; ++mt)
-#pragma unroll
-      for (int r = 0; r < 4; ++r) {
-        int rb = mt * 16 + lg * 4 + r;
-        unsigned byteoff = (unsigned)rb * 1024u
-                         + (((unsigned)j * 2u) ^ (((unsigned)rb & 7u) << 4));
-        *(u16t*)((char*)hm_l + byteoff) = f2bf(ftanh(acc[mt][r] + bias));
-      }
-  }
-  __syncthreads();
-
-#pragma unroll
-  for (int nt = 0; nt < 4; ++nt) {
-    int d0 = (wv * 4 + nt) * 16;
-    f4 acc[5];
-#pragma unroll
-    for (int mt = 0; mt < 5; ++mt) acc[mt] = (f4){0,0,0,0};
-#pragma unroll 2
-    for (int kk = 0; kk < 16; ++kk) {
-      bf8 b = *(const bf8*)(mw2W + (size_t)(d0 + lr) * 512 + kk * 32 + koff);
-#pragma unroll
-      for (int mt = 0; mt < 5; ++mt) {
-        int rb = mt * 16 + lr;
-        unsigned byteoff = (unsigned)rb * 1024u
-                         + (((unsigned)(kk * 64 + lg * 16)) ^ (((unsigned)rb & 7u) << 4));
-        bf8 a = *(const bf8*)((const char*)hm_l + byteoff);
-        acc[mt] = MFMA16(a, b, acc[mt]);
-      }
-    }
-    int d = d0 + lr;
-    float bias = mb2[m * EMBED + d];
-#pragma unroll
-    for (int mt = 0; mt < 5; ++mt)
-#pragma unroll
-      for (int r = 0; r < 4; ++r) {
-        int rb = mt * 16 + lg * 4 + r;
-        float v = ftanh(acc[mt][r] + bias);
-        mat_l[rb * 1024 + d] = (signed char)__float2int_rn(v * 127.f);
-      }
-  }
-  __syncthreads();
-
-  {
-    signed char* matB = mat_g + (size_t)pid0 * 20480;
-#pragma unroll
-    for (int i = 0; i < 5; ++i) {
-      int off = i * 16384 + tid * 16;
-      int4 sv = *(const int4*)(mat_l + off);
-      int4 ov;
-      if (m > 0) ov = *(const int4*)(matB + off);
-      const signed char* svb = (const signed char*)&sv;
-      const signed char* ovb = (const signed char*)&ov;
-      int4 res;
-      signed char* rsb = (signed char*)&res;
-#pragma unroll
-      for (int b = 0; b < 16; ++b) {
-        float v = (float)svb[b] * (1.f / 127.f);
-        float mo = (m == 0) ? 1.f : (float)ovb[b] * (1.f / 127.f);
-        float mn = fminf(fmaxf(v + mo, -1.f), 1.f);
-        rsb[b] = (signed char)__float2int_rn(mn * 127.f);
-      }
-      *(int4*)(matB + off) = res;
-    }
-  }
-}
-
-__global__ __launch_bounds__(1024) void simenc_valu(
-    const float* __restrict__ img_emb, const float* __restrict__ cap_emb,
-    const float* __restrict__ alv_w,  const float* __restrict__ alv_b,
-    const float* __restrict__ rar_qw, const float* __restrict__ rar_qb,
-    const float* __restrict__ rar_kw, const float* __restrict__ rar_kb,
-    const float* __restrict__ rar_vw, const float* __restrict__ rar_vb,
-    const float* __restrict__ sw1, const float* __restrict__ sb1,
-    const float* __restrict__ sw2, const float* __restrict__ sb2,
-    const float* __restrict__ mw1, const float* __restrict__ mb1,
-    const float* __restrict__ mw2, const float* __restrict__ mb2,
-    const float* __restrict__ eval_w, const float* __restrict__ eval_b,
-    float* __restrict__ out)
-{
-  __shared__ float buf[NWORD * EMBED];
-  __shared__ float smid[NWORD * SIMDIM];
-  __shared__ float attn_raw[NREG * NWORD];
-  __shared__ float attnT[NWORD * NREG];
-  __shared__ float smoothq[NWORD];
-  __shared__ float sim_hig[SIMDIM];
-  __shared__ float hqu[SIMDIM];
-  __shared__ float wsm_[NWORD];
-  __shared__ float red[16 * NWORD];
-  __shared__ float rq[NWORD];
-  __shared__ float ssig;
-
-  const int tid = threadIdx.x;
-  const int lane = tid & 63;
-  const int wv = tid >> 6;
-  const int pair = blockIdx.x;
-  const int img = pair & 63;
-  const int cap = pair >> 6;
-  const float* ctx = img_emb + (size_t)img * (NREG * EMBED);
-  const float* qry = cap_emb + (size_t)cap * (NWORD * EMBED);
-
-  float mat[NWORD];
-#pragma unroll
-  for (int q = 0; q < NWORD; ++q) mat[q] = 1.f;
-  if (tid < NWORD) smoothq[tid] = 9.f;
-  __syncthreads();
-
-  for (int m = 0; m < 3; ++m) {
-#pragma unroll 4
-    for (int q = 0; q < NWORD; ++q)
-      buf[q * EMBED + tid] = qry[q * EMBED + tid] * mat[q];
-    __syncthreads();
-    if (tid < NWORD * NREG) {
-      int q = tid / NREG, s = tid % NREG;
-      const float4* c4 = (const float4*)(ctx + s * EMBED);
-      const float4* q4 = (const float4*)(buf + q * EMBED);
-      float acc = 0.f;
-#pragma unroll 4
-      for (int i = 0; i < EMBED / 4; ++i) acc += d4(c4[i], q4[i]);
-      attn_raw[s * NWORD + q] = (acc > 0.f) ? acc : 0.1f * acc;
-    }
-    __syncthreads();
-    if (tid < NREG) {
-      int s = tid; float sumsq = 0.f;
-#pragma unroll
-      for (int q = 0; q < NWORD; ++q) { float v = attn_raw[s * NWORD + q]; sumsq += v * v; }
-      float sc = 1.f / (sqrtf(sumsq) + EPS);
-#pragma unroll
-      for (int q = 0; q < NWORD; ++q) attnT[q * NREG + s] = attn_raw[s * NWORD + q] * sc;
-    }
-    __syncthreads();
-    if (tid < NWORD) {
-      int q = tid; float sm = smoothq[q]; float mx = -1e30f;
-      for (int s = 0; s < NREG; ++s) mx = fmaxf(mx, attnT[q * NREG + s] * sm);
-      float sum = 0.f;
-      for (int s = 0; s < NREG; ++s) { float e = __expf(attnT[q * NREG + s] * sm - mx); attnT[q * NREG + s] = e; sum += e; }
-      float r = 1.f / sum;
-      for (int s = 0; s < NREG; ++s) attnT[q * NREG + s] *= r;
-    }
-    __syncthreads();
-    {
-      float wacc[NWORD];
-#pragma unroll
-      for (int q = 0; q < NWORD; ++q) wacc[q] = 0.f;
-#pragma unroll
-      for (int sc_ = 0; sc_ < 3; ++sc_) {
-        float c[12];
-#pragma unroll
-        for (int i = 0; i < 12; ++i) c[i] = ctx[(sc_ * 12 + i) * EMBED + tid];
-#pragma unroll
-        for (int q = 0; q < NWORD; ++q) {
-          const float4* a4 = (const float4*)(attnT + q * NREG + sc_ * 12);
-          float4 a0 = a4[0], a1 = a4[1], a2 = a4[2];
-          wacc[q] += a0.x*c[0] + a0.y*c[1] + a0.z*c[2] + a0.w*c[3]
-                   + a1.x*c[4] + a1.y*c[5] + a1.z*c[6] + a1.w*c[7]
-                   + a2.x*c[8] + a2.y*c[9] + a2.z*c[10] + a2.w*c[11];
-        }
-      }
-#pragma unroll
-      for (int q = 0; q < NWORD; ++q) {
-        float v = wsum(wacc[q] * wacc[q]);
-        if (lane == 0) red[wv * NWORD + q] = v;
-      }
-      __syncthreads();
-      if (tid < NWORD) {
-        float s = 0.f;
-#pragma unroll
-        for (int w = 0; w < 16; ++w) s += red[w * NWORD + tid];
-        rq[tid] = 1.f / (sqrtf(s) + EPS);
-      }
-      __syncthreads();
-#pragma unroll 4
-      for (int q = 0; q < NWORD; ++q) {
-        float wn = wacc[q] * rq[q];
-        float t = qry[q * EMBED + tid] - wn;
-        buf[q * EMBED + tid] = t * t;
-      }
-    }
-    __syncthreads();
-    {
-      int t = tid & 255, g = tid >> 8;
-      const float4* w4 = (const float4*)(alv_w + ((size_t)m * SIMDIM + t) * EMBED);
-      float acc[5] = {0, 0, 0, 0, 0};
-      for (int i = 0; i < EMBED / 4; ++i) {
-        float4 w = w4[i];
-#pragma unroll
-        for (int k = 0; k < 5; ++k) acc[k] += d4(w, ((const float4*)(buf + (g + 4 * k) * EMBED))[i]);
-      }
-      float b = alv_b[m * SIMDIM + t];
-#pragma unroll
-      for (int k = 0; k < 5; ++k) smid[(g + 4 * k) * SIMDIM + t] = acc[k] + b;
-    }
-    __syncthreads();
-#pragma unroll
-    for (int rep = 0; rep < 2; ++rep) {
-      int q = wv + rep * 16;
-      if (q < NWORD) {
-        float4 v = ((const float4*)(smid + q * SIMDIM))[lane];
-        float s = wsum(d4(v, v));
-        if (lane == 0) rq[q] = 1.f / (sqrtf(s) + EPS);
-      }
-    }
-    __syncthreads();
-#pragma unroll
-    for (int k = 0; k < 5; ++k) { int e = tid + k * 1024; smid[e] *= rq[e >> 8]; }
-    __syncthreads();
-    if (m == 0 && tid < SIMDIM) {
-      float s = 0.f;
-#pragma unroll
-      for (int q = 0; q < NWORD; ++q) s += smid[q * SIMDIM + tid];
-      sim_hig[tid] = s * (1.f / NWORD);
-    }
-    __syncthreads();
-    if (m < 2) {
-      {
-        int j = tid & 511, g = tid >> 9;
-        const float4* w4 = (const float4*)(mw1 + ((size_t)m * H1 + j) * SIMDIM);
-        float acc[10];
-#pragma unroll
-        for (int k = 0; k < 10; ++k) acc[k] = 0.f;
-        for (int i = 0; i < SIMDIM / 4; ++i) {
-          float4 w = w4[i];
-#pragma unroll
-          for (int k = 0; k < 10; ++k) acc[k] += d4(w, ((const float4*)(smid + (g + 2 * k) * SIMDIM))[i]);
-        }
-        float b = mb1[m * H1 + j];
-#pragma unroll
-        for (int k = 0; k < 10; ++k) buf[(g + 2 * k) * H1 + j] = ftanh(acc[k] + b);
-      }
-      __syncthreads();
-      {
-        const float4* w4 = (const float4*)(mw2 + ((size_t)m * EMBED + tid) * H1);
-        float acc[NWORD];
-#pragma unroll
-        for (int q = 0; q < NWORD; ++q) acc[q] = 0.f;
-        for (int i = 0; i < H1 / 4; ++i) {
-          float4 w = w4[i];
-#pragma unroll
-          for (int q = 0; q < NWORD; ++q) acc[q] += d4(w, ((const float4*)(buf + q * H1))[i]);
-        }
-        float b = mb2[m * EMBED + tid];
-#pragma unroll
-        for (int q = 0; q < NWORD; ++q)
-          mat[q] = fminf(fmaxf(ftanh(acc[q] + b) + mat[q], -1.f), 1.f);
-      }
-      {
-        int j = tid & 127, g = tid >> 7;
-        const float4* w4 = (const float4*)(sw1 + ((size_t)m * HSD + j) * SIMDIM);
-        float a0 = 0.f, a1 = 0.f, a2 = 0.f;
-        for (int i = 0; i < SIMDIM / 4; ++i) {
-          float4 w = w4[i];
-          a0 += d4(w, ((const float4*)(smid + g * SIMDIM))[i]);
-          a1 += d4(w, ((const float4*)(smid + (g + 8) * SIMDIM))[i]);
-          if (g < 4) a2 += d4(w, ((const float4*)(smid + (g + 16) * SIMDIM))[i]);
-        }
-        float b = sb1[m * HSD + j];
-        buf[10240 + g * HSD + j] = ftanh(a0 + b);
-        buf[10240 + (g + 8) * HSD + j] = ftanh(a1 + b);
-        if (g < 4) buf[10240 + (g + 16) * HSD + j] = ftanh(a2 + b);
-      }
-      __syncthreads();
-      {
-        const float* sw2m = sw2 + m * HSD;
-#pragma unroll
-        for (int rep = 0; rep < 2; ++rep) {
-          int q = wv + rep * 16;
-          if (q < NWORD) {
-            float v = buf[10240 + q * HSD + lane] * sw2m[lane]
-                    + buf[10240 + q * HSD + 64 + lane] * sw2m[64 + lane];
-            v = wsum(v);
-            if (lane == 0) smoothq[q] = fmaxf(0.f, v + sb2[m] + smoothq[q]);
-          }
-        }
-      }
-      __syncthreads();
-    }
-    {
-      int t = tid & 255, g = tid >> 8;
-      const float4* w4 = (const float4*)(rar_kw + ((size_t)m * SIMDIM + t) * SIMDIM);
-      float acc[5] = {0, 0, 0, 0, 0};
-      for (int i = 0; i < SIMDIM / 4; ++i) {
-        float4 w = w4[i];
-#pragma unroll
-        for (int k = 0; k < 5; ++k) acc[k] += d4(w, ((const float4*)(smid + (g + 4 * k) * SIMDIM))[i]);
-      }
-      float b = rar_kb[m * SIMDIM + t];
-#pragma unroll
-      for (int k = 0; k < 5; ++k) buf[12800 + (g + 4 * k) * SIMDIM + t] = ftanh(acc[k] + b);
-    }
-    if (tid < SIMDIM) {
-      const float4* w4 = (const float4*)(rar_qw + ((size_t)m * SIMDIM + tid) * SIMDIM);
-      const float4* s4 = (const float4*)sim_hig;
-      float acc = 0.f;
-      for (int i = 0; i < SIMDIM / 4; ++i) acc += d4(w4[i], s4[i]);
-      hqu[tid] = ftanh(acc + rar_qb[m * SIMDIM + tid]) * rar_vw[m * SIMDIM + tid];
-    }
-    __syncthreads();
-#pragma unroll
-    for (int rep = 0; rep < 2; ++rep) {
-      int q = wv + rep * 16;
-      if (q < NWORD) {
-        float4 a = ((const float4*)(buf + 12800 + q * SIMDIM))[lane];
-        float4 u = ((const float4*)hqu)[lane];
-        float v = wsum(d4(a, u));
-        if (lane == 0) red[q] = v + rar_vb[m];
-      }
-    }
-    __syncthreads();
-    if (tid < 64) {
-      float v = (tid < NWORD) ? red[tid] : -1e30f;
-      float mx = wmax(v);
-      float e = (tid < NWORD) ? __expf(v - mx) : 0.f;
-      float s = wsum(e);
-      if (tid < NWORD) wsm_[tid] = e / s;
-    }
-    __syncthreads();
-    if (tid < SIMDIM) {
-      float acc = 0.f;
-#pragma unroll
-      for (int q = 0; q < NWORD; ++q) acc += wsm_[q] * smid[q * SIMDIM + tid];
-      sim_hig[tid] = acc;
-    }
-    __syncthreads();
-    if (tid < 64) {
-      float4 v = ((const float4*)sim_hig)[tid];
-      float s = wsum(d4(v, v));
-      if (tid == 0) ssig = 1.f / (sqrtf(s) + EPS);
-    }
-    __syncthreads();
-    if (tid < SIMDIM) sim_hig[tid] *= ssig;
-    __syncthreads();
-  }
-  if (tid < 64) {
-    float4 s4v = ((const float4*)sim_hig)[tid];
-    float4 w4v = ((const float4*)eval_w)[tid];
-    float v = wsum(d4(s4v, w4v));
-    if (tid == 0) out[img * NCAP + cap] = 1.f / (1.f + __expf(-(v + eval_b[0])));
-  }
-}
-
 extern "C" void kernel_launch(void* const* d_in, const int* in_sizes, int n_in,
                               void* d_out, int out_size, void* d_ws, size_t ws_size,
                               hipStream_t stream) {
   (void)in_sizes; (void)n_in; (void)out_size;
   u16t* ws = (u16t*)d_ws;
 
-  if (ws_size >= (size_t)WS_FULL_BYTES) {
-    cvt_kernel<<<2048, 1024, 0, stream>>>(
-        (const float*)d_in[3],  (const float*)d_in[7],  (const float*)d_in[15],
-        (const float*)d_in[17], (const float*)d_in[11], (const float*)d_in[0], ws);
-    ctxt_kernel<<<1024, 256, 0, stream>>>((const float*)d_in[0], ws + WS_CTXT);
-
-    signed char* mat_g = (signed char*)d_ws + OFFB_MAT;
-    u16t*  smid_g   = (u16t*)((char*)d_ws + OFFB_SMID);
-    float* shig_g   = (float*)((char*)d_ws + OFFB_SHIG);
-    float* smooth_g = (float*)((char*)d_ws + OFFB_SMOOTH);
+  signed char* mat_g = (signed char*)d_ws + OFFB_MAT;
+  u16t*  smid_g   = (u16t*)((char*)d_ws + OFFB_SMID);
+  float* shig_g   = (float*)((char*)d_ws + OFFB_SHIG);
+  float* smooth_g = (float*)((char*)d_ws + OFFB_SMOOTH);
+
+  cvt_kernel<<<2048, 1024, 0, stream>>>(
+      (const float*)d_in[3],  (const float*)d_in[7],  (const float*)d_in[15],
+      (const float*)d_in[17], (const float*)d_in[11], (const float*)d_in[0], ws);
+  ctxt_kernel<<<1024, 256, 0, stream>>>((const float*)d_in[0], ws + WS_CTXT);
+
+  if (ws_size >= (size_t)WS_FULL2_BYTES) {
+    u16t*  srep_g   = (u16t*)((char*)d_ws + OFFB_SREP);
+    float* hqu_g    = (float*)((char*)d_ws + OFFB_HQU);
+    float* logits_g = (float*)((char*)d_ws + OFFB_LOG);
 
     for (int m = 0; m < 3; ++m) {
-      simenc_k1<<<NIMG * NCAP, 512, 0, stream>>>(
+      simenc_ka<<<NIMG * NCAP, 512, 0, stream>>>(
+          (const float*)d_in[1], ws, mat_g, smooth_g, srep_g, m);
+      simenc_kf<<<NIMG * NCAP / 4, 1024, 0, stream>>>(
+          (const float*)d_in[4], ws, srep_g, smid_g, shig_g, m);
+      simenc_kh<<<1024, 1024, 0, stream>>>(
+          (const float*)d_in[5], (const float*)d_in[6], (const float*)d_in[9],
+          shig_g, hqu_g, m);
+      simenc_kr<<<NIMG * NCAP / 4, 1024, 0, stream>>>(
+          (const float*)d_in[8], (const float*)d_in[10],
+          (const float*)d_in[12], (const float*)d_in[13], (const float*)d_in[14],
+          ws, smid_g, hqu_g, logits_g, smooth_g, m);
+      simenc_ki<<<NIMG * NCAP, 256, 0, stream>>>(
+          (const float*)d_in[19], (const float*)d_in[20],
+          smid_g, logits_g, shig_g, (float*)d_out, m);
+      if (m < 2)
+        simenc_k2<<<NIMG * NCAP / 4, 1024, 0, stream>>>(
+            (const float*)d_in[16], (const float*)d_in[18],
+            ws, smid_g, mat_g, m);
+    }
+  } else {
+    for (int m = 0; m < 3; ++m) {
+      simenc_k1f<<<NIMG * NCAP, 512, 0, stream>>>(
           (const float*)d_in[1],  (const float*)d_in[4],
           (const float*)d_in[5],  (const float*)d_in[6],  (const float*)d_in[8],
           (const float*)d_in[9],  (const float*)d_in[10],
@@ -912,18 +1107,5 @@
             (const float*)d_in[16], (const float*)d_in[18],
             ws, smid_g, mat_g, m);
     }
-  } else {
-    simenc_valu<<<NIMG * NCAP, 1024, 0, stream>>>(
-        (const float*)d_in[0],  (const float*)d_in[1],
-        (const float*)d_in[3],  (const float*)d_in[4],
-        (const float*)d_in[5],  (const float*)d_in[6],
-        (const float*)d_in[7],  (const float*)d_in[8],
-        (const float*)d_in[9],  (const float*)d_in[10],
-        (const float*)d_in[11], (const float*)d_in[12],
-        (const float*)d_in[13], (const float*)d_in[14],
-        (const float*)d_in[15], (const float*)d_in[16],
-        (const float*)d_in[17], (const float*)d_in[18],
-        (const float*)d_in[19], (const float*)d_in[20],
-        (float*)d_out);
-  }
-}
+  }
+}
```

New measurement: 3.513 ms. No clear change (-0.1%).
